# Optimization experiments

Hardware: AMD Instinct MI355X
Metric: run time of the kernel (lower is better)

Reference implementation:

```python
import jax, jax.numpy as jnp
import numpy as np
import math

C = 8  # sparsity factor c from __init__


def setup_inputs() -> dict:
    key = jax.random.key(0)
    kq, kk, kv, ki = jax.random.split(key, 4)
    B, Q, KV, D = 4, 2048, 2048, 512
    U = int(Q * math.log(KV))  # 15615 sampled keys, matches torch _sampler
    q = jax.random.normal(kq, (B, Q, D), dtype=jnp.float32)
    k = jax.random.normal(kk, (B, KV, D), dtype=jnp.float32)
    v = jax.random.normal(kv, (B, KV, D), dtype=jnp.float32)
    sample_idx = jax.random.randint(ki, (B, U), 0, KV)  # per-batch random key sample
    return {"q": q, "k": k, "v": v, "sample_idx": sample_idx}


def reference(q, k, v, sample_idx):
    B, Q, D = q.shape
    KV = k.shape[1]
    u = int(C * math.log(Q))  # number of selected queries (== 60 here)

    # _sampler: gather sampled keys per batch -> (B, U, D)
    k_bar = jnp.take_along_axis(k, sample_idx[:, :, None], axis=1)

    # sparsity measure M = max_j s_bar - mean_j s_bar, s_bar: (B, Q, U)
    s_bar = jnp.einsum('bqd,bud->bqu', q, k_bar)
    M = s_bar.max(axis=2) - s_bar.mean(axis=2)  # (B, Q)

    # top-u queries per batch
    _, top_idx = jax.lax.top_k(M, u)  # (B, u)
    q_bar = jnp.take_along_axis(q, top_idx[:, :, None], axis=1)  # (B, u, D)

    # small dense attention over full keys; NOTE: original scales by sqrt(kv_len)
    attn = jnp.einsum('bud,bkd->buk', q_bar, k) / jnp.sqrt(jnp.asarray(KV, q.dtype))
    attn = jax.nn.softmax(attn, axis=-1)
    s1 = jnp.einsum('buk,bkd->bud', attn, v)  # (B, u, D)

    # fill all positions with mean of v, then scatter attention outputs
    s = jnp.broadcast_to(v.mean(axis=1, keepdims=True), q.shape)  # (B, Q, D)
    bidx = jnp.arange(B)[:, None]
    s = s.at[bidx, top_idx].set(s1)
    return s
```

## Files before the change

### kernel.cpp

```cpp
#include <hip/hip_runtime.h>
#include <math.h>

#define BATCH 4
#define QN    2048
#define KVN   2048
#define DN    512
#define U_TOT 15615
#define NSEL  60
#define NSLOT 32
#define S1KS  64
#define CPART 8

typedef __attribute__((ext_vector_type(8))) short bf16x8;
typedef __attribute__((ext_vector_type(4))) float f32x4;

__device__ __forceinline__ unsigned short f2bf(float f) {
  unsigned u = __float_as_uint(f);
  unsigned r = (u + 0x7fffu + ((u >> 16) & 1u)) >> 16;
  return (unsigned short)r;
}
__device__ __forceinline__ float bf2f(unsigned short h) {
  return __uint_as_float(((unsigned)h) << 16);
}
__device__ __forceinline__ void gld16(const void* g, void* l) {
  __builtin_amdgcn_global_load_lds(
      (const __attribute__((address_space(1))) unsigned int*)g,
      (__attribute__((address_space(3))) unsigned int*)l, 16, 0, 0);
}

__global__ __launch_bounds__(256) void prep_kernel(
    const float* __restrict__ q, const float* __restrict__ k,
    unsigned short* __restrict__ qhi, unsigned short* __restrict__ qlo,
    unsigned short* __restrict__ khi, unsigned short* __restrict__ klo,
    const int* __restrict__ sidx, float* __restrict__ cntp,
    float* __restrict__ vmean, int* __restrict__ rowslot)
{
  __shared__ int h[KVN];
  const int bid = blockIdx.x;
  const int t = threadIdx.x;

  if (bid < 8192) {
    const int half = bid >> 12;
    const int i = (bid & 4095) * 256 + t;
    const float* in = half ? k : q;
    unsigned short* hi = half ? khi : qhi;
    unsigned short* lo = half ? klo : qlo;
    float4 f = reinterpret_cast<const float4*>(in)[i];
    ushort4 hh, ll;
    hh.x = f2bf(f.x); ll.x = f2bf(f.x - bf2f(hh.x));
    hh.y = f2bf(f.y); ll.y = f2bf(f.y - bf2f(hh.y));
    hh.z = f2bf(f.z); ll.z = f2bf(f.z - bf2f(hh.z));
    hh.w = f2bf(f.w); ll.w = f2bf(f.w - bf2f(hh.w));
    reinterpret_cast<ushort4*>(hi)[i] = hh;
    reinterpret_cast<ushort4*>(lo)[i] = ll;
  } else if (bid < 8224) {
    const int cb = bid - 8192;
    const int b  = cb >> 3;
    const int p  = cb & 7;
    for (int i = t; i < KVN; i += 256) h[i] = 0;
    __syncthreads();
    const int start = p * 1952;
    const int end   = (start + 1952 < U_TOT) ? start + 1952 : U_TOT;
    for (int i = start + t; i < end; i += 256) atomicAdd(&h[sidx[b * U_TOT + i]], 1);
    __syncthreads();
    for (int i = t; i < KVN; i += 256)
      cntp[((size_t)(p * BATCH + b)) * KVN + i] = (float)h[i];
  } else if (bid == 8224) {
    for (int i = t; i < BATCH * DN; i += 256) vmean[i] = 0.f;
  } else {
    const int idx = (bid - 8225) * 256 + t;
    rowslot[idx] = -1;
  }
}

__global__ __launch_bounds__(256) void s_mfma_kernel(
    const unsigned short* __restrict__ qh, const unsigned short* __restrict__ ql,
    const unsigned short* __restrict__ kh, const unsigned short* __restrict__ kl,
    const float* __restrict__ cntp, float* __restrict__ Pmax, float* __restrict__ Psum)
{
  __shared__ unsigned short Ah[128 * 32];
  __shared__ unsigned short Al[128 * 32];
  __shared__ unsigned short Bh[128 * 32];
  __shared__ unsigned short Bl[128 * 32];
  __shared__ float cnt_s[128];

  const int t = threadIdx.x;
  const int w = t >> 6;
  const int L = t & 63;
  const int mbase = (w & 1) * 64;
  const int nbase = (w >> 1) * 64;
  const int lm = L & 15;

  const int bid = blockIdx.x;
  const int xcd = bid & 7;
  const int idx = bid >> 3;
  const int b   = xcd >> 1;
  const int ji  = (xcd & 1) * 8 + (idx >> 3);
  const int qi0 = (idx & 7) * 2;
  const int j0  = ji * 128;

  if (t < 128) {
    float c = 0.f;
#pragma unroll
    for (int p = 0; p < CPART; ++p)
      c += cntp[((size_t)(p * BATCH + b)) * KVN + j0 + t];
    cnt_s[t] = c;
  }

  const int srow = t >> 2;
  const int schk = (t & 3) ^ ((t >> 3) & 3);

  const int perm  = (L >> 4) ^ ((lm >> 1) & 3);
  const int abase = (mbase * 4 + lm * 4 + perm) * 8;
  const int bbase = (nbase * 4 + lm * 4 + perm) * 8;

  const size_t koff0 = ((size_t)(b * KVN) + j0 + srow) * DN + (size_t)(schk * 8);
  const size_t koff1 = koff0 + (size_t)64 * DN;

  for (int qq = 0; qq < 2; ++qq) {
    const int q0 = (qi0 + qq) * 128;
    const size_t qoff0 = ((size_t)(b * QN) + q0 + srow) * DN + (size_t)(schk * 8);
    const size_t qoff1 = qoff0 + (size_t)64 * DN;

    f32x4 acc[4][4];
#pragma unroll
    for (int nf = 0; nf < 4; ++nf)
#pragma unroll
      for (int mf = 0; mf < 4; ++mf) {
        acc[nf][mf][0] = 0.f; acc[nf][mf][1] = 0.f;
        acc[nf][mf][2] = 0.f; acc[nf][mf][3] = 0.f;
      }

    for (int d0 = 0; d0 < DN; d0 += 32) {
      __syncthreads();
      gld16(qh + qoff0 + d0, &Ah[t * 8]);
      gld16(qh + qoff1 + d0, &Ah[(t + 256) * 8]);
      gld16(ql + qoff0 + d0, &Al[t * 8]);
      gld16(ql + qoff1 + d0, &Al[(t + 256) * 8]);
      gld16(kh + koff0 + d0, &Bh[t * 8]);
      gld16(kh + koff1 + d0, &Bh[(t + 256) * 8]);
      gld16(kl + koff0 + d0, &Bl[t * 8]);
      gld16(kl + koff1 + d0, &Bl[(t + 256) * 8]);
      __syncthreads();

      bf16x8 ah[4], al[4];
#pragma unroll
      for (int mf = 0; mf < 4; ++mf) {
        ah[mf] = *reinterpret_cast<const bf16x8*>(&Ah[abase + mf * 512]);
        al[mf] = *reinterpret_cast<const bf16x8*>(&Al[abase + mf * 512]);
      }
#pragma unroll
      for (int nf = 0; nf < 4; ++nf) {
        bf16x8 bh = *reinterpret_cast<const bf16x8*>(&Bh[bbase + nf * 512]);
        bf16x8 bl = *reinterpret_cast<const bf16x8*>(&Bl[bbase + nf * 512]);
#pragma unroll
        for (int mf = 0; mf < 4; ++mf) {
          acc[nf][mf] = __builtin_amdgcn_mfma_f32_16x16x32_bf16(ah[mf], bh, acc[nf][mf], 0, 0, 0);
          acc[nf][mf] = __builtin_amdgcn_mfma_f32_16x16x32_bf16(ah[mf], bl, acc[nf][mf], 0, 0, 0);
          acc[nf][mf] = __builtin_amdgcn_mfma_f32_16x16x32_bf16(al[mf], bh, acc[nf][mf], 0, 0, 0);
        }
      }
    }

    float mx[4][4], wsm[4][4];
#pragma unroll
    for (int mf = 0; mf < 4; ++mf)
#pragma unroll
      for (int r = 0; r < 4; ++r) { mx[mf][r] = -INFINITY; wsm[mf][r] = 0.f; }

#pragma unroll
    for (int nf = 0; nf < 4; ++nf) {
      const float c = cnt_s[nbase + nf * 16 + lm];
      const bool has = (c > 0.f);
#pragma unroll
      for (int mf = 0; mf < 4; ++mf)
#pragma unroll
        for (int r = 0; r < 4; ++r) {
          const float v = acc[nf][mf][r];
          if (has) mx[mf][r] = fmaxf(mx[mf][r], v);
          wsm[mf][r] = fmaf(c, v, wsm[mf][r]);
        }
    }

    const size_t spi = (size_t)((ji * 2 + (w >> 1)) * BATCH + b);
#pragma unroll
    for (int mf = 0; mf < 4; ++mf)
#pragma unroll
      for (int r = 0; r < 4; ++r) {
        float m = mx[mf][r], s = wsm[mf][r];
#pragma unroll
        for (int o = 1; o < 16; o <<= 1) {
          m = fmaxf(m, __shfl_xor(m, o));
          s += __shfl_xor(s, o);
        }
        if (lm == 0) {
          const int qrow = q0 + mbase + mf * 16 + (L >> 4) * 4 + r;
          Pmax[spi * QN + qrow] = m;
          Psum[spi * QN + qrow] = s;
        }
      }
  }
}

__global__ __launch_bounds__(256) void select_kernel(
    const float* __restrict__ Pmax, const float* __restrict__ Psum,
    int* __restrict__ topidx, int* __restrict__ rowslot)
{
  const int b = blockIdx.x;
  const int t = threadIdx.x;
  unsigned long long key[8];
#pragma unroll
  for (int s = 0; s < 8; ++s) {
    const int qq = s * 256 + t;
    float m = -INFINITY, sm = 0.f;
#pragma unroll 4
    for (int p = 0; p < NSLOT; ++p) {
      m = fmaxf(m, Pmax[((size_t)(p * BATCH + b)) * QN + qq]);
      sm += Psum[((size_t)(p * BATCH + b)) * QN + qq];
    }
    const float M = m - sm * (1.0f / (float)U_TOT);
    unsigned u = __float_as_uint(M);
    u = (u & 0x80000000u) ? ~u : (u | 0x80000000u);
    key[s] = ((unsigned long long)u << 32) | (unsigned)(QN - qq);
  }

  __shared__ unsigned hist[256];
  __shared__ unsigned long long pref_s;
  __shared__ unsigned rank_s;
  __shared__ unsigned cnt_s;
  if (t == 0) { pref_s = 0ull; rank_s = NSEL; cnt_s = 0u; }
  __syncthreads();

  for (int level = 7; level >= 0; --level) {
    const int shift = level * 8;
    hist[t] = 0;
    __syncthreads();
    const unsigned long long pref = pref_s;
    const unsigned rank = rank_s;
#pragma unroll
    for (int s = 0; s < 8; ++s) {
      const bool match = (level == 7) || ((key[s] >> (shift + 8)) == pref);
      if (match) atomicAdd(&hist[(unsigned)((key[s] >> shift) & 255u)], 1u);
    }
    __syncthreads();
    if (t < 64) {
      const unsigned h0 = hist[4 * t], h1 = hist[4 * t + 1];
      const unsigned h2 = hist[4 * t + 2], h3 = hist[4 * t + 3];
      const unsigned loc = h0 + h1 + h2 + h3;
      unsigned run = loc;
#pragma unroll
      for (int o = 1; o < 64; o <<= 1) {
        const unsigned oth = (unsigned)__shfl_down((int)run, o);
        if (t + o < 64) run += oth;
      }
      const unsigned suf = run - loc;
      const unsigned c3 = suf, c2 = c3 + h3, c1 = c2 + h2, c0 = c1 + h1;
      int hit = -1; unsigned cgt = 0;
      if      (c3 < rank && rank <= c3 + h3) { hit = 4 * t + 3; cgt = c3; }
      else if (c2 < rank && rank <= c2 + h2) { hit = 4 * t + 2; cgt = c2; }
      else if (c1 < rank && rank <= c1 + h1) { hit = 4 * t + 1; cgt = c1; }
      else if (c0 < rank && rank <= c0 + h0) { hit = 4 * t + 0; cgt = c0; }
      if (hit >= 0) {
        pref_s = ((level == 7) ? 0ull : (pref_s << 8)) | (unsigned long long)(unsigned)hit;
        rank_s = rank - cgt;
      }
    }
    __syncthreads();
  }

  const unsigned long long T = pref_s;
#pragma unroll
  for (int s = 0; s < 8; ++s) {
    if (key[s] >= T) {
      const unsigned pos = atomicAdd(&cnt_s, 1u);
      const int qsel = QN - (int)(key[s] & 0xFFFFFFFFull);
      topidx[b * 64 + pos] = qsel;
      rowslot[b * QN + qsel] = (int)pos;
    }
  }
}

#define SBM 64
#define SBN 32
#define SBK 32
__global__ __launch_bounds__(256) void scores_kernel(
    const float* __restrict__ q, const int* __restrict__ topidx,
    const float* __restrict__ k, float* __restrict__ attn)
{
  __shared__ float a_s[SBK][SBM + 4];
  __shared__ float b_s[SBK][SBN + 4];
  __shared__ int tix_s[64];
  const int t  = threadIdx.x;
  const int tx = t & 7;
  const int ty = t >> 3;
  const int kv0 = blockIdx.x * SBN;
  const int b   = blockIdx.y;
  const float* kb = k + (size_t)b * KVN * DN;

  if (t < 64) tix_s[t] = (t < NSEL) ? topidx[b * 64 + t] : 0;
  __syncthreads();

  float acc[2][4];
#pragma unroll
  for (int i = 0; i < 2; ++i)
#pragma unroll
    for (int j = 0; j < 4; ++j) acc[i][j] = 0.f;

  const int c4 = (t & 7) * 4;
  const int r0 = t >> 3;
  const int srow0 = tix_s[r0];
  const int srow1 = tix_s[r0 + 32];

  for (int d0 = 0; d0 < DN; d0 += SBK) {
#pragma unroll
    for (int rr = 0; rr < 2; ++rr) {
      int row = r0 + rr * 32;
      int srow = rr ? srow1 : srow0;
      float4 av = *reinterpret_cast<const float4*>(q + ((size_t)(b * QN) + srow) * DN + d0 + c4);
      a_s[c4 + 0][row] = av.x; a_s[c4 + 1][row] = av.y;
      a_s[c4 + 2][row] = av.z; a_s[c4 + 3][row] = av.w;
    }
    {
      float4 bv = *reinterpret_cast<const float4*>(kb + (size_t)(kv0 + r0) * DN + d0 + c4);
      b_s[c4 + 0][r0] = bv.x; b_s[c4 + 1][r0] = bv.y;
      b_s[c4 + 2][r0] = bv.z; b_s[c4 + 3][r0] = bv.w;
    }
    __syncthreads();
#pragma unroll
    for (int kk = 0; kk < SBK; ++kk) {
      const float a0 = a_s[kk][ty * 2];
      const float a1 = a_s[kk][ty * 2 + 1];
      float4 bv = *reinterpret_cast<const float4*>(&b_s[kk][tx * 4]);
      float bf[4] = {bv.x, bv.y, bv.z, bv.w};
#pragma unroll
      for (int j = 0; j < 4; ++j) {
        acc[0][j] = fmaf(a0, bf[j], acc[0][j]);
        acc[1][j] = fmaf(a1, bf[j], acc[1][j]);
      }
    }
    __syncthreads();
  }

#pragma unroll
  for (int i = 0; i < 2; ++i) {
    int j = ty * 2 + i;
    if (j < NSEL) {
      float4 o = make_float4(acc[i][0], acc[i][1], acc[i][2], acc[i][3]);
      *reinterpret_cast<float4*>(attn + ((size_t)(b * NSEL + j)) * KVN + kv0 + tx * 4) = o;
    }
  }
}

__global__ __launch_bounds__(256) void softmax_kernel(float* __restrict__ attn)
{
  __shared__ float buf[KVN];
  __shared__ float wred[4];
  const int t = threadIdx.x;
  const int L = t & 63, wv = t >> 6;
  float* row = attn + (size_t)blockIdx.x * KVN;

  float m = -INFINITY;
  for (int i = t; i < KVN; i += 256) { float v = row[i]; buf[i] = v; m = fmaxf(m, v); }
#pragma unroll
  for (int o = 1; o < 64; o <<= 1) m = fmaxf(m, __shfl_xor(m, o));
  if (L == 0) wred[wv] = m;
  __syncthreads();
  m = fmaxf(fmaxf(wred[0], wred[1]), fmaxf(wred[2], wred[3]));

  const float sc = 0.022097086912079608f;
  float s = 0.f;
  for (int i = t; i < KVN; i += 256) { float e = __expf((buf[i] - m) * sc); buf[i] = e; s += e; }
#pragma unroll
  for (int o = 1; o < 64; o <<= 1) s += __shfl_xor(s, o);
  __syncthreads();
  if (L == 0) wred[wv] = s;
  __syncthreads();
  const float inv = 1.f / (wred[0] + wred[1] + wred[2] + wred[3]);
  for (int i = t; i < KVN; i += 256) row[i] = buf[i] * inv;
}

__global__ __launch_bounds__(256) void s1_partial_kernel(
    const float* __restrict__ attn, const float* __restrict__ v,
    float* __restrict__ part, float* __restrict__ vmean)
{
  __shared__ float a_s[32][61];
  const int t    = threadIdx.x;
  const int dv4  = t & 63;
  const int jg   = t >> 6;
  const int dh   = blockIdx.x;
  const int b    = blockIdx.y;
  const int ks   = blockIdx.z;
  const int kv0  = ks * 32;
  const int dbase = dh * 256 + dv4 * 4;

  for (int x = t; x < NSEL * 32; x += 256) {
    const int j = x >> 5, kk = x & 31;
    a_s[kk][j] = attn[((size_t)(b * NSEL + j)) * KVN + kv0 + kk];
  }
  __syncthreads();

  f32x4 acc[15];
#pragma unroll
  for (int i = 0; i < 15; ++i) { acc[i][0] = 0.f; acc[i][1] = 0.f; acc[i][2] = 0.f; acc[i][3] = 0.f; }
  f32x4 vsum; vsum[0] = 0.f; vsum[1] = 0.f; vsum[2] = 0.f; vsum[3] = 0.f;

  const float* vb = v + ((size_t)b * KVN + kv0) * DN + dbase;
#pragma unroll 8
  for (int kk = 0; kk < 32; ++kk) {
    const f32x4 vv = *reinterpret_cast<const f32x4*>(vb + (size_t)kk * DN);
    if (jg == 0) { vsum[0] += vv[0]; vsum[1] += vv[1]; vsum[2] += vv[2]; vsum[3] += vv[3]; }
#pragma unroll
    for (int jj = 0; jj < 15; ++jj) {
      const float a = a_s[kk][jg * 15 + jj];
      acc[jj][0] = fmaf(a, vv[0], acc[jj][0]);
      acc[jj][1] = fmaf(a, vv[1], acc[jj][1]);
      acc[jj][2] = fmaf(a, vv[2], acc[jj][2]);
      acc[jj][3] = fmaf(a, vv[3], acc[jj][3]);
    }
  }

#pragma unroll
  for (int jj = 0; jj < 15; ++jj) {
    const int j = jg * 15 + jj;
    *reinterpret_cast<f32x4*>(
        part + ((size_t)((ks * BATCH + b) * NSEL) + j) * DN + dbase) = acc[jj];
  }
  if (jg == 0) {
    float* vm = vmean + (size_t)b * DN + dbase;
    atomicAdd(vm + 0, vsum[0]);
    atomicAdd(vm + 1, vsum[1]);
    atomicAdd(vm + 2, vsum[2]);
    atomicAdd(vm + 3, vsum[3]);
  }
}

__global__ __launch_bounds__(256) void out_kernel(
    const float* __restrict__ part, const float* __restrict__ vmean,
    const int* __restrict__ rowslot, float* __restrict__ out)
{
  const int gid = blockIdx.x * 256 + threadIdx.x;
  const int d4 = gid & 127;
  const int qq = (gid >> 7) & (QN - 1);
  const int b  = gid >> 18;
  const int slot = rowslot[b * QN + qq];
  f32x4 o;
  if (slot >= 0) {
    o[0] = 0.f; o[1] = 0.f; o[2] = 0.f; o[3] = 0.f;
    for (int ks = 0; ks < S1KS; ++ks) {
      const f32x4 p = reinterpret_cast<const f32x4*>(part)[
          ((size_t)((ks * BATCH + b) * NSEL) + slot) * (DN / 4) + d4];
      o[0] += p[0]; o[1] += p[1]; o[2] += p[2]; o[3] += p[3];
    }
  } else {
    const f32x4 vm = reinterpret_cast<const f32x4*>(vmean)[b * (DN / 4) + d4];
    const float sc = 1.0f / (float)KVN;
    o[0] = vm[0] * sc; o[1] = vm[1] * sc; o[2] = vm[2] * sc; o[3] = vm[3] * sc;
  }
  reinterpret_cast<f32x4*>(out)[gid] = o;
}

extern "C" void kernel_launch(void* const* d_in, const int* in_sizes, int n_in,
                              void* d_out, int out_size, void* d_ws, size_t ws_size,
                              hipStream_t stream) {
  const float* q    = (const float*)d_in[0];
  const float* k    = (const float*)d_in[1];
  const float* v    = (const float*)d_in[2];
  const int*   sidx = (const int*)d_in[3];
  float* out = (float*)d_out;
  char*  W   = (char*)d_ws;

  const size_t NEL = (size_t)BATCH * QN * DN;
  unsigned short* qh = (unsigned short*)W;
  unsigned short* ql = qh + NEL;
  unsigned short* kh = ql + NEL;
  unsigned short* kl = kh + NEL;

  float* attn  = (float*)W;
  float* part  = (float*)(W + 2097152);
  float* vmean = (float*)(W + 34078720);

  char* W2 = W + 37748736;
  float* cntp    = (float*)W2;
  float* Pmax    = (float*)(W2 + 262144);
  float* Psum    = (float*)(W2 + 262144 + 1048576);
  int*   topidx  = (int*)(W2 + 262144 + 2097152);
  int*   rowslot = (int*)(W2 + 262144 + 2097152 + 4096);

  prep_kernel<<<dim3(8257), 256, 0, stream>>>(q, k, qh, ql, kh, kl, sidx, cntp, vmean, rowslot);
  s_mfma_kernel<<<dim3(512), 256, 0, stream>>>(qh, ql, kh, kl, cntp, Pmax, Psum);
  select_kernel<<<dim3(BATCH), 256, 0, stream>>>(Pmax, Psum, topidx, rowslot);
  scores_kernel<<<dim3(KVN / SBN, BATCH), 256, 0, stream>>>(q, topidx, k, attn);
  softmax_kernel<<<dim3(BATCH * NSEL), 256, 0, stream>>>(attn);
  s1_partial_kernel<<<dim3(2, BATCH, S1KS), 256, 0, stream>>>(attn, v, part, vmean);
  out_kernel<<<dim3(4096), 256, 0, stream>>>(part, vmean, rowslot, out);
}
```

Baseline: 238.6 us.

## Fuse scores, softmax and PV into split-KV flash-style kernel with rescaled merge

```diff
diff --git a/kernel.cpp b/kernel.cpp
--- a/kernel.cpp
+++ b/kernel.cpp
@@ -8,8 +8,7 @@
 #define U_TOT 15615
 #define NSEL  60
 #define NSLOT 32
-#define S1KS  64
-#define CPART 8
+#define KVCH  64
 
 typedef __attribute__((ext_vector_type(8))) short bf16x8;
 typedef __attribute__((ext_vector_type(4))) float f32x4;
@@ -32,7 +31,7 @@
     const float* __restrict__ q, const float* __restrict__ k,
     unsigned short* __restrict__ qhi, unsigned short* __restrict__ qlo,
     unsigned short* __restrict__ khi, unsigned short* __restrict__ klo,
-    const int* __restrict__ sidx, float* __restrict__ cntp,
+    const int* __restrict__ sidx, float* __restrict__ cnt,
     float* __restrict__ vmean, int* __restrict__ rowslot)
 {
   __shared__ int h[KVN];
@@ -53,22 +52,17 @@
     hh.w = f2bf(f.w); ll.w = f2bf(f.w - bf2f(hh.w));
     reinterpret_cast<ushort4*>(hi)[i] = hh;
     reinterpret_cast<ushort4*>(lo)[i] = ll;
-  } else if (bid < 8224) {
-    const int cb = bid - 8192;
-    const int b  = cb >> 3;
-    const int p  = cb & 7;
+  } else if (bid < 8196) {
+    const int b = bid - 8192;
     for (int i = t; i < KVN; i += 256) h[i] = 0;
     __syncthreads();
-    const int start = p * 1952;
-    const int end   = (start + 1952 < U_TOT) ? start + 1952 : U_TOT;
-    for (int i = start + t; i < end; i += 256) atomicAdd(&h[sidx[b * U_TOT + i]], 1);
-    __syncthreads();
-    for (int i = t; i < KVN; i += 256)
-      cntp[((size_t)(p * BATCH + b)) * KVN + i] = (float)h[i];
-  } else if (bid == 8224) {
+    for (int i = t; i < U_TOT; i += 256) atomicAdd(&h[sidx[b * U_TOT + i]], 1);
+    __syncthreads();
+    for (int i = t; i < KVN; i += 256) cnt[b * KVN + i] = (float)h[i];
+  } else if (bid == 8196) {
     for (int i = t; i < BATCH * DN; i += 256) vmean[i] = 0.f;
   } else {
-    const int idx = (bid - 8225) * 256 + t;
+    const int idx = (bid - 8197) * 256 + t;
     rowslot[idx] = -1;
   }
 }
@@ -76,7 +70,7 @@
 __global__ __launch_bounds__(256) void s_mfma_kernel(
     const unsigned short* __restrict__ qh, const unsigned short* __restrict__ ql,
     const unsigned short* __restrict__ kh, const unsigned short* __restrict__ kl,
-    const float* __restrict__ cntp, float* __restrict__ Pmax, float* __restrict__ Psum)
+    const float* __restrict__ cnt, float* __restrict__ Pmax, float* __restrict__ Psum)
 {
   __shared__ unsigned short Ah[128 * 32];
   __shared__ unsigned short Al[128 * 32];
@@ -99,13 +93,7 @@
   const int qi0 = (idx & 7) * 2;
   const int j0  = ji * 128;
 
-  if (t < 128) {
-    float c = 0.f;
-#pragma unroll
-    for (int p = 0; p < CPART; ++p)
-      c += cntp[((size_t)(p * BATCH + b)) * KVN + j0 + t];
-    cnt_s[t] = c;
-  }
+  if (t < 128) cnt_s[t] = cnt[b * KVN + j0 + t];
 
   const int srow = t >> 2;
   const int schk = (t & 3) ^ ((t >> 3) & 3);
@@ -280,42 +268,44 @@
   }
 }
 
-#define SBM 64
-#define SBN 32
-#define SBK 32
-__global__ __launch_bounds__(256) void scores_kernel(
+__global__ __launch_bounds__(256) void attn_kernel(
     const float* __restrict__ q, const int* __restrict__ topidx,
-    const float* __restrict__ k, float* __restrict__ attn)
+    const float* __restrict__ k, const float* __restrict__ v,
+    float* __restrict__ part, float* __restrict__ mstat, float* __restrict__ lstat,
+    float* __restrict__ vmean)
 {
-  __shared__ float a_s[SBK][SBM + 4];
-  __shared__ float b_s[SBK][SBN + 4];
+  __shared__ float a_s[32][68];
+  __shared__ float b_s[32][36];
+  __shared__ float e_s[32][65];
   __shared__ int tix_s[64];
+
   const int t  = threadIdx.x;
+  const int ch = blockIdx.x;
+  const int b  = blockIdx.y;
+  const int kv0 = ch * 32;
+  const float* kb = k + (size_t)b * KVN * DN;
+
+  if (t < 64) tix_s[t] = (t < NSEL) ? topidx[b * 64 + t] : topidx[b * 64];
+  __syncthreads();
+
   const int tx = t & 7;
   const int ty = t >> 3;
-  const int kv0 = blockIdx.x * SBN;
-  const int b   = blockIdx.y;
-  const float* kb = k + (size_t)b * KVN * DN;
-
-  if (t < 64) tix_s[t] = (t < NSEL) ? topidx[b * 64 + t] : 0;
-  __syncthreads();
-
-  float acc[2][4];
-#pragma unroll
-  for (int i = 0; i < 2; ++i)
-#pragma unroll
-    for (int j = 0; j < 4; ++j) acc[i][j] = 0.f;
-
   const int c4 = (t & 7) * 4;
   const int r0 = t >> 3;
   const int srow0 = tix_s[r0];
   const int srow1 = tix_s[r0 + 32];
 
-  for (int d0 = 0; d0 < DN; d0 += SBK) {
+  float acc[2][4];
+#pragma unroll
+  for (int i = 0; i < 2; ++i)
+#pragma unroll
+    for (int j = 0; j < 4; ++j) acc[i][j] = 0.f;
+
+  for (int d0 = 0; d0 < DN; d0 += 32) {
 #pragma unroll
     for (int rr = 0; rr < 2; ++rr) {
-      int row = r0 + rr * 32;
-      int srow = rr ? srow1 : srow0;
+      const int row = r0 + rr * 32;
+      const int srow = rr ? srow1 : srow0;
       float4 av = *reinterpret_cast<const float4*>(q + ((size_t)(b * QN) + srow) * DN + d0 + c4);
       a_s[c4 + 0][row] = av.x; a_s[c4 + 1][row] = av.y;
       a_s[c4 + 2][row] = av.z; a_s[c4 + 3][row] = av.w;
@@ -327,7 +317,7 @@
     }
     __syncthreads();
 #pragma unroll
-    for (int kk = 0; kk < SBK; ++kk) {
+    for (int kk = 0; kk < 32; ++kk) {
       const float a0 = a_s[kk][ty * 2];
       const float a1 = a_s[kk][ty * 2 + 1];
       float4 bv = *reinterpret_cast<const float4*>(&b_s[kk][tx * 4]);
@@ -341,101 +331,75 @@
     __syncthreads();
   }
 
+  const float sc = 0.022097086912079608f;
 #pragma unroll
   for (int i = 0; i < 2; ++i) {
-    int j = ty * 2 + i;
-    if (j < NSEL) {
-      float4 o = make_float4(acc[i][0], acc[i][1], acc[i][2], acc[i][3]);
-      *reinterpret_cast<float4*>(attn + ((size_t)(b * NSEL + j)) * KVN + kv0 + tx * 4) = o;
-    }
-  }
-}
-
-__global__ __launch_bounds__(256) void softmax_kernel(float* __restrict__ attn)
-{
-  __shared__ float buf[KVN];
-  __shared__ float wred[4];
-  const int t = threadIdx.x;
-  const int L = t & 63, wv = t >> 6;
-  float* row = attn + (size_t)blockIdx.x * KVN;
-
-  float m = -INFINITY;
-  for (int i = t; i < KVN; i += 256) { float v = row[i]; buf[i] = v; m = fmaxf(m, v); }
-#pragma unroll
-  for (int o = 1; o < 64; o <<= 1) m = fmaxf(m, __shfl_xor(m, o));
-  if (L == 0) wred[wv] = m;
+    const int row = ty * 2 + i;
+    float m = fmaxf(fmaxf(acc[i][0], acc[i][1]), fmaxf(acc[i][2], acc[i][3]));
+#pragma unroll
+    for (int o = 1; o < 8; o <<= 1) m = fmaxf(m, __shfl_xor(m, o));
+    float e0 = __expf((acc[i][0] - m) * sc);
+    float e1 = __expf((acc[i][1] - m) * sc);
+    float e2 = __expf((acc[i][2] - m) * sc);
+    float e3 = __expf((acc[i][3] - m) * sc);
+    float l = e0 + e1 + e2 + e3;
+#pragma unroll
+    for (int o = 1; o < 8; o <<= 1) l += __shfl_xor(l, o);
+    e_s[tx * 4 + 0][row] = e0;
+    e_s[tx * 4 + 1][row] = e1;
+    e_s[tx * 4 + 2][row] = e2;
+    e_s[tx * 4 + 3][row] = e3;
+    if (tx == 0) {
+      mstat[((size_t)(ch * BATCH + b)) * 64 + row] = m;
+      lstat[((size_t)(ch * BATCH + b)) * 64 + row] = l;
+    }
+  }
   __syncthreads();
-  m = fmaxf(fmaxf(wred[0], wred[1]), fmaxf(wred[2], wred[3]));
-
-  const float sc = 0.022097086912079608f;
-  float s = 0.f;
-  for (int i = t; i < KVN; i += 256) { float e = __expf((buf[i] - m) * sc); buf[i] = e; s += e; }
-#pragma unroll
-  for (int o = 1; o < 64; o <<= 1) s += __shfl_xor(s, o);
-  __syncthreads();
-  if (L == 0) wred[wv] = s;
-  __syncthreads();
-  const float inv = 1.f / (wred[0] + wred[1] + wred[2] + wred[3]);
-  for (int i = t; i < KVN; i += 256) row[i] = buf[i] * inv;
-}
-
-__global__ __launch_bounds__(256) void s1_partial_kernel(
-    const float* __restrict__ attn, const float* __restrict__ v,
-    float* __restrict__ part, float* __restrict__ vmean)
-{
-  __shared__ float a_s[32][61];
-  const int t    = threadIdx.x;
-  const int dv4  = t & 63;
-  const int jg   = t >> 6;
-  const int dh   = blockIdx.x;
-  const int b    = blockIdx.y;
-  const int ks   = blockIdx.z;
-  const int kv0  = ks * 32;
-  const int dbase = dh * 256 + dv4 * 4;
-
-  for (int x = t; x < NSEL * 32; x += 256) {
-    const int j = x >> 5, kk = x & 31;
-    a_s[kk][j] = attn[((size_t)(b * NSEL + j)) * KVN + kv0 + kk];
-  }
-  __syncthreads();
-
-  f32x4 acc[15];
-#pragma unroll
-  for (int i = 0; i < 15; ++i) { acc[i][0] = 0.f; acc[i][1] = 0.f; acc[i][2] = 0.f; acc[i][3] = 0.f; }
-  f32x4 vsum; vsum[0] = 0.f; vsum[1] = 0.f; vsum[2] = 0.f; vsum[3] = 0.f;
-
-  const float* vb = v + ((size_t)b * KVN + kv0) * DN + dbase;
+
+  const int dv4 = t & 63;
+  const int jg  = t >> 6;
+  const float* vb = v + ((size_t)b * KVN + kv0) * DN;
+
+#pragma unroll
+  for (int dh = 0; dh < 2; ++dh) {
+    const int dbase = dh * 256 + dv4 * 4;
+    f32x4 po[15];
+#pragma unroll
+    for (int i = 0; i < 15; ++i) { po[i][0] = 0.f; po[i][1] = 0.f; po[i][2] = 0.f; po[i][3] = 0.f; }
+    f32x4 vsum; vsum[0] = 0.f; vsum[1] = 0.f; vsum[2] = 0.f; vsum[3] = 0.f;
+
 #pragma unroll 8
-  for (int kk = 0; kk < 32; ++kk) {
-    const f32x4 vv = *reinterpret_cast<const f32x4*>(vb + (size_t)kk * DN);
-    if (jg == 0) { vsum[0] += vv[0]; vsum[1] += vv[1]; vsum[2] += vv[2]; vsum[3] += vv[3]; }
+    for (int kk = 0; kk < 32; ++kk) {
+      const f32x4 vv = *reinterpret_cast<const f32x4*>(vb + (size_t)kk * DN + dbase);
+      if (jg == 0) { vsum[0] += vv[0]; vsum[1] += vv[1]; vsum[2] += vv[2]; vsum[3] += vv[3]; }
+#pragma unroll
+      for (int jj = 0; jj < 15; ++jj) {
+        const float a = e_s[kk][jg * 15 + jj];
+        po[jj][0] = fmaf(a, vv[0], po[jj][0]);
+        po[jj][1] = fmaf(a, vv[1], po[jj][1]);
+        po[jj][2] = fmaf(a, vv[2], po[jj][2]);
+        po[jj][3] = fmaf(a, vv[3], po[jj][3]);
+      }
+    }
 #pragma unroll
     for (int jj = 0; jj < 15; ++jj) {
-      const float a = a_s[kk][jg * 15 + jj];
-      acc[jj][0] = fmaf(a, vv[0], acc[jj][0]);
-      acc[jj][1] = fmaf(a, vv[1], acc[jj][1]);
-      acc[jj][2] = fmaf(a, vv[2], acc[jj][2]);
-      acc[jj][3] = fmaf(a, vv[3], acc[jj][3]);
-    }
-  }
-
-#pragma unroll
-  for (int jj = 0; jj < 15; ++jj) {
-    const int j = jg * 15 + jj;
-    *reinterpret_cast<f32x4*>(
-        part + ((size_t)((ks * BATCH + b) * NSEL) + j) * DN + dbase) = acc[jj];
-  }
-  if (jg == 0) {
-    float* vm = vmean + (size_t)b * DN + dbase;
-    atomicAdd(vm + 0, vsum[0]);
-    atomicAdd(vm + 1, vsum[1]);
-    atomicAdd(vm + 2, vsum[2]);
-    atomicAdd(vm + 3, vsum[3]);
+      const int row = jg * 15 + jj;
+      *reinterpret_cast<f32x4*>(
+          part + (((size_t)(ch * BATCH + b)) * 64 + row) * DN + dbase) = po[jj];
+    }
+    if (jg == 0) {
+      float* vm = vmean + (size_t)b * DN + dbase;
+      atomicAdd(vm + 0, vsum[0]);
+      atomicAdd(vm + 1, vsum[1]);
+      atomicAdd(vm + 2, vsum[2]);
+      atomicAdd(vm + 3, vsum[3]);
+    }
   }
 }
 
 __global__ __launch_bounds__(256) void out_kernel(
-    const float* __restrict__ part, const float* __restrict__ vmean,
+    const float* __restrict__ part, const float* __restrict__ mstat,
+    const float* __restrict__ lstat, const float* __restrict__ vmean,
     const int* __restrict__ rowslot, float* __restrict__ out)
 {
   const int gid = blockIdx.x * 256 + threadIdx.x;
@@ -445,16 +409,26 @@
   const int slot = rowslot[b * QN + qq];
   f32x4 o;
   if (slot >= 0) {
+    const float sc = 0.022097086912079608f;
+    float M = -INFINITY;
+    for (int ch = 0; ch < KVCH; ++ch)
+      M = fmaxf(M, mstat[((size_t)(ch * BATCH + b)) * 64 + slot]);
+    float L = 0.f;
     o[0] = 0.f; o[1] = 0.f; o[2] = 0.f; o[3] = 0.f;
-    for (int ks = 0; ks < S1KS; ++ks) {
+    for (int ch = 0; ch < KVCH; ++ch) {
+      const float w = __expf((mstat[((size_t)(ch * BATCH + b)) * 64 + slot] - M) * sc);
+      L += w * lstat[((size_t)(ch * BATCH + b)) * 64 + slot];
       const f32x4 p = reinterpret_cast<const f32x4*>(part)[
-          ((size_t)((ks * BATCH + b) * NSEL) + slot) * (DN / 4) + d4];
-      o[0] += p[0]; o[1] += p[1]; o[2] += p[2]; o[3] += p[3];
-    }
+          (((size_t)(ch * BATCH + b)) * 64 + slot) * (DN / 4) + d4];
+      o[0] = fmaf(w, p[0], o[0]); o[1] = fmaf(w, p[1], o[1]);
+      o[2] = fmaf(w, p[2], o[2]); o[3] = fmaf(w, p[3], o[3]);
+    }
+    const float inv = 1.f / L;
+    o[0] *= inv; o[1] *= inv; o[2] *= inv; o[3] *= inv;
   } else {
     const f32x4 vm = reinterpret_cast<const f32x4*>(vmean)[b * (DN / 4) + d4];
-    const float sc = 1.0f / (float)KVN;
-    o[0] = vm[0] * sc; o[1] = vm[1] * sc; o[2] = vm[2] * sc; o[3] = vm[3] * sc;
+    const float sc2 = 1.0f / (float)KVN;
+    o[0] = vm[0] * sc2; o[1] = vm[1] * sc2; o[2] = vm[2] * sc2; o[3] = vm[3] * sc2;
   }
   reinterpret_cast<f32x4*>(out)[gid] = o;
 }
@@ -474,23 +448,21 @@
   unsigned short* ql = qh + NEL;
   unsigned short* kh = ql + NEL;
   unsigned short* kl = kh + NEL;
-
-  float* attn  = (float*)W;
-  float* part  = (float*)(W + 2097152);
-  float* vmean = (float*)(W + 34078720);
+  float* part = (float*)W;
 
   char* W2 = W + 37748736;
-  float* cntp    = (float*)W2;
-  float* Pmax    = (float*)(W2 + 262144);
-  float* Psum    = (float*)(W2 + 262144 + 1048576);
-  int*   topidx  = (int*)(W2 + 262144 + 2097152);
-  int*   rowslot = (int*)(W2 + 262144 + 2097152 + 4096);
-
-  prep_kernel<<<dim3(8257), 256, 0, stream>>>(q, k, qh, ql, kh, kl, sidx, cntp, vmean, rowslot);
-  s_mfma_kernel<<<dim3(512), 256, 0, stream>>>(qh, ql, kh, kl, cntp, Pmax, Psum);
+  float* cnt     = (float*)W2;
+  float* Pmax    = (float*)(W2 + 32768);
+  float* Psum    = (float*)(W2 + 32768 + 1048576);
+  int*   topidx  = (int*)(W2 + 2129920);
+  int*   rowslot = (int*)(W2 + 2134016);
+  float* vmean   = (float*)(W2 + 2166784);
+  float* mstat   = (float*)(W2 + 2174976);
+  float* lstat   = (float*)(W2 + 2240512);
+
+  prep_kernel<<<dim3(8229), 256, 0, stream>>>(q, k, qh, ql, kh, kl, sidx, cnt, vmean, rowslot);
+  s_mfma_kernel<<<dim3(512), 256, 0, stream>>>(qh, ql, kh, kl, cnt, Pmax, Psum);
   select_kernel<<<dim3(BATCH), 256, 0, stream>>>(Pmax, Psum, topidx, rowslot);
-  scores_kernel<<<dim3(KVN / SBN, BATCH), 256, 0, stream>>>(q, topidx, k, attn);
-  softmax_kernel<<<dim3(BATCH * NSEL), 256, 0, stream>>>(attn);
-  s1_partial_kernel<<<dim3(2, BATCH, S1KS), 256, 0, stream>>>(attn, v, part, vmean);
-  out_kernel<<<dim3(4096), 256, 0, stream>>>(part, vmean, rowslot, out);
-}
+  attn_kernel<<<dim3(KVCH, BATCH), 256, 0, stream>>>(q, topidx, k, v, part, mstat, lstat, vmean);
+  out_kernel<<<dim3(4096), 256, 0, stream>>>(part, mstat, lstat, vmean, rowslot, out);
+}
```

After: 275.3 us. +15.4%, slower.
